# Performance work log

Hardware: AMD Instinct MI355X
Metric: run time of the kernel (lower is better)

Reference implementation:

```python
import jax, jax.numpy as jnp
import numpy as np

EMBED = 256

def _resize(x, h, w):
    # bilinear, half-pixel centers == torch align_corners=False
    B, C = x.shape[:2]
    return jax.image.resize(x, (B, C, h, w), method='bilinear')

def _conv(x, w, b, pad):
    y = jax.lax.conv_general_dilated(x, w, (1, 1), [(pad, pad), (pad, pad)],
                                     dimension_numbers=('NCHW', 'OIHW', 'NCHW'))
    return y + b[None, :, None, None]

def _box1d(x, r, axis):
    # windowed sum over [i-r, i+r], window clipped at borders
    x = jnp.moveaxis(x, axis, -1)
    n = x.shape[-1]
    c = jnp.cumsum(x, axis=-1)
    idx = jnp.arange(n)
    hi = c[..., jnp.clip(idx + r, 0, n - 1)]
    lo_i = idx - r - 1
    lo = jnp.where(lo_i >= 0, c[..., jnp.clip(lo_i, 0, n - 1)], 0.0)
    return jnp.moveaxis(hi - lo, -1, axis)

def _box_mean(x, r):
    # mean filter over (2r+1)^2 window, normalized by valid pixel count at borders
    H, W = x.shape[-2:]
    s = _box1d(_box1d(x, r, -2), r, -1)
    ch = _box1d(jnp.ones((H,), x.dtype), r, 0)
    cw = _box1d(jnp.ones((W,), x.dtype), r, 0)
    return s / (ch[:, None] * cw[None, :])

def _guided_filter(I, p, r, eps):
    # He et al. guided filter. I: (H,W) guide, p: (C,H,W) src, vectorized over C
    mean_I = _box_mean(I, r)
    var_I = _box_mean(I * I, r) - mean_I ** 2
    mean_p = _box_mean(p, r)
    cov_Ip = _box_mean(I[None] * p, r) - mean_I[None] * mean_p
    a = cov_Ip / (var_I[None] + eps)
    b = mean_p - a * mean_I[None]
    return _box_mean(a, r) * I[None] + _box_mean(b, r)

def _forward(fg, bg, mask, feat, w1, b1, w2, b2, w3, b3, wm, bm):
    h2, w2d = 2 * mask.shape[2], 2 * mask.shape[3]
    mask_2x_raw = _resize(mask, h2, w2d)
    feat_2x_raw = _resize(feat, h2, w2d)
    fg_2x = _resize(fg, h2, w2d)
    bg_2x = _resize(bg, h2, w2d)
    x = jnp.concatenate((mask_2x_raw, fg_2x, bg_2x, feat_2x_raw), axis=1)
    x = jax.nn.relu(_conv(x, w1, b1, 0))
    feat_2x = jax.nn.relu(_conv(x, w2, b2, 2))
    guide = jnp.mean(fg_2x, axis=1)[0] * 128.0  # (H2, W2)
    r = int(0.01 * h2)  # static shape -> python int, jit-safe
    filt = _guided_filter(guide, feat_2x[0], r, 0.01)[None]  # (1,C,H2,W2)
    feat_2x = jax.nn.relu(_conv(filt, w3, b3, 0))
    mask_2x = jax.nn.sigmoid(_conv(feat_2x, wm, bm, 0))
    return mask_2x, feat_2x

def setup_inputs():
    key = jax.random.key(0)
    ks = jax.random.split(key, 8)
    E = EMBED
    return {
        'fg': jax.random.normal(ks[0], (1, 3, 128, 128), jnp.float32),
        'bg': jax.random.normal(ks[1], (1, 3, 128, 128), jnp.float32),
        'mask': jax.random.uniform(ks[2], (1, 1, 128, 128), dtype=jnp.float32),
        'feat': jax.random.normal(ks[3], (1, E, 128, 128), jnp.float32),
        'w1': jax.random.normal(ks[4], (E, E + 7, 1, 1), jnp.float32) * 0.05,
        'b1': jnp.zeros((E,), jnp.float32),
        'w2': jax.random.normal(ks[5], (E, E, 5, 5), jnp.float32) * 0.02,
        'b2': jnp.zeros((E,), jnp.float32),
        'w3': jax.random.normal(ks[6], (E, E, 1, 1), jnp.float32) * 0.05,
        'b3': jnp.zeros((E,), jnp.float32),
        'wm': jax.random.normal(ks[7], (1, E, 1, 1), jnp.float32) * 0.05,
        'bm': jnp.zeros((1,), jnp.float32),
    }

def reference(fg, bg, mask, feat, w1, b1, w2, b2, w3, b3, wm, bm):
    return _forward(fg, bg, mask, feat, w1, b1, w2, b2, w3, b3, wm, bm)
```

## Files before the change

### kernel.cpp

```cpp
#include <hip/hip_runtime.h>
#include <hip/hip_bf16.h>
#include <hip/hip_fp16.h>
#include <math.h>


#define P2 65536
#define PADW 260

typedef short  frag8  __attribute__((ext_vector_type(8)));
typedef float  f32x4  __attribute__((ext_vector_type(4)));

__device__ __forceinline__ void load16_lds(const void* gsrc, void* lds) {
    __builtin_amdgcn_global_load_lds((const __attribute__((address_space(1))) void*)gsrc,
                                     (__attribute__((address_space(3))) void*)lds, 16, 0, 0);
}

struct BilC { int y0, y1, x0, x1; float wy0, wy1, wx0, wx1; };
__device__ __forceinline__ BilC bil_coords(int oy, int ox) {
    BilC c;
    int m = oy >> 1;
    if ((oy & 1) == 0) { c.y0 = (m > 0) ? m - 1 : 0; c.y1 = m; c.wy0 = 0.25f; }
    else               { c.y0 = m; c.y1 = (m < 127) ? m + 1 : 127; c.wy0 = 0.75f; }
    c.wy1 = 1.0f - c.wy0;
    int n = ox >> 1;
    if ((ox & 1) == 0) { c.x0 = (n > 0) ? n - 1 : 0; c.x1 = n; c.wx0 = 0.25f; }
    else               { c.x0 = n; c.x1 = (n < 127) ? n + 1 : 127; c.wx0 = 0.75f; }
    c.wx1 = 1.0f - c.wx0;
    return c;
}
__device__ __forceinline__ float bil_eval(const float* __restrict__ src, const BilC& c) {
    return c.wy0 * (c.wx0 * src[c.y0 * 128 + c.x0] + c.wx1 * src[c.y0 * 128 + c.x1])
         + c.wy1 * (c.wx0 * src[c.y1 * 128 + c.x0] + c.wx1 * src[c.y1 * 128 + c.x1]);
}

__global__ void upsample_x(const float* __restrict__ mask, const float* __restrict__ fg,
                           const float* __restrict__ bg, const float* __restrict__ feat,
                           __hip_bfloat16* __restrict__ xp) {
    int p = blockIdx.x * 256 + threadIdx.x;
    int chunk = blockIdx.y;
    union { __hip_bfloat16 h[8]; f32x4 v; } u;
    if (chunk >= 33) {
        f32x4 z = {0.f, 0.f, 0.f, 0.f};
        *(f32x4*)&xp[((size_t)chunk * P2 + p) * 8] = z;
        return;
    }
    BilC bc = bil_coords(p >> 8, p & 255);
#pragma unroll
    for (int j = 0; j < 8; j++) {
        int c = chunk * 8 + j;
        float v = 0.f;
        if (c < 263) {
            const float* src = (c == 0) ? mask
                             : (c < 4)  ? fg + (c - 1) * 16384
                             : (c < 7)  ? bg + (c - 4) * 16384
                             :            feat + (c - 7) * 16384;
            v = bil_eval(src, bc);
        }
        u.h[j] = __float2bfloat16(v);
    }
    *(f32x4*)&xp[((size_t)chunk * P2 + p) * 8] = u.v;
}

__global__ __launch_bounds__(256) void guide_stats(const float* __restrict__ fg,
                                                   float* __restrict__ guide,
                                                   float* __restrict__ meanI,
                                                   float* __restrict__ varI) {
    __shared__ float G[20 * 21];
    int tid = threadIdx.x;
    int gx0 = blockIdx.x * 16, gy0 = blockIdx.y * 16;
    for (int i = tid; i < 400; i += 256) {
        int r = i / 20, c = i - r * 20;
        int gy = gy0 + r - 2, gx = gx0 + c - 2;
        float v = 0.f;
        if ((unsigned)gy < 256u && (unsigned)gx < 256u) {
            BilC bc = bil_coords(gy, gx);
            v = (bil_eval(fg, bc) + bil_eval(fg + 16384, bc) + bil_eval(fg + 32768, bc))
                * (128.0f / 3.0f);
        }
        G[r * 21 + c] = v;
    }
    __syncthreads();
    int ty = tid >> 4, tx = tid & 15;
    int gy = gy0 + ty, gx = gx0 + tx;
    float s = 0.f, ss = 0.f;
#pragma unroll
    for (int dy = 0; dy < 5; dy++)
#pragma unroll
        for (int dx = 0; dx < 5; dx++) {
            float v = G[(ty + dy) * 21 + tx + dx];
            s += v; ss += v * v;
        }
    int cy = ((gy + 2 < 255) ? gy + 2 : 255) - ((gy - 2 > 0) ? gy - 2 : 0) + 1;
    int cx = ((gx + 2 < 255) ? gx + 2 : 255) - ((gx - 2 > 0) ? gx - 2 : 0) + 1;
    float inv = 1.0f / (float)(cy * cx);
    float m = s * inv;
    guide[gy * 256 + gx] = G[(ty + 2) * 21 + tx + 2];
    meanI[gy * 256 + gx] = m;
    varI[gy * 256 + gx]  = ss * inv - m * m;
}

__global__ void prep_all(const float* __restrict__ w2, const float* __restrict__ w1,
                         const float* __restrict__ w3,
                         __hip_bfloat16* __restrict__ wpk2, __hip_bfloat16* __restrict__ wpk1,
                         __hip_bfloat16* __restrict__ wpk3, __hip_bfloat16* __restrict__ y1p,
                         float* __restrict__ haccum) {
    int b = blockIdx.x;
    int tid = threadIdx.x;
    if (b < 129) {
        int idx = b * 256 + tid;
        if (idx >= 33024) return;
        int pid = idx >> 4, chunk = idx & 15;
        int py, px;
        if (pid < 520)       { py = pid / 260;               px = pid - (py) * 260; }
        else if (pid < 1040) { int t = pid - 520; int r = t / 260; py = 258 + r; px = t - r * 260; }
        else                 { int t = pid - 1040; int r = t >> 2; int c = t & 3;
                               py = 2 + r; px = (c < 2) ? c : 256 + c; }
        f32x4 z = {0.f, 0.f, 0.f, 0.f};
        f32x4* dst = (f32x4*)&y1p[((size_t)py * PADW + px) * 256 + chunk * 16];
        dst[0] = z; dst[1] = z;
    } else if (b < 193) {
        int idx = (b - 193 + 64) * 256 + tid - 64 * 256;
        idx = (b - 129) * 256 + tid;
        f32x4 z = {0.f, 0.f, 0.f, 0.f};
        *(f32x4*)&haccum[idx * 4] = z;
    } else if (b < 993) {
        int idx = (b - 193) * 256 + tid;
        int lane = idx & 63;
        int nb = (idx >> 6) & 15;
        int t2 = idx >> 10;
        int tap = t2 % 25, ict = t2 / 25;
        int oc = nb * 16 + (lane & 15);
        int ic0 = ict * 32 + (lane >> 4) * 8;
        union { __hip_bfloat16 h[8]; f32x4 v; } u;
#pragma unroll
        for (int j = 0; j < 8; j++)
            u.h[j] = __float2bfloat16(w2[(oc * 256 + ic0 + j) * 25 + tap]);
        *(f32x4*)&wpk2[(size_t)idx * 8] = u.v;
    } else {
        const float* W; __hip_bfloat16* dst; int K, KT, idx;
        if (b < 1029) { W = w1; dst = wpk1; K = 263; KT = 9; idx = (b - 993) * 256 + tid; }
        else          { W = w3; dst = wpk3; K = 256; KT = 8; idx = (b - 1029) * 256 + tid; }
        if (idx >= KT * 16 * 64) return;
        int lane = idx & 63;
        int nbg = (idx >> 6) & 15;
        int kt = idx >> 10;
        int oc = nbg * 16 + (lane & 15);
        int ic0 = kt * 32 + (lane >> 4) * 8;
        union { __hip_bfloat16 h[8]; f32x4 v; } u;
#pragma unroll
        for (int j = 0; j < 8; j++) {
            int ic = ic0 + j;
            u.h[j] = (ic < K) ? __float2bfloat16(W[(size_t)oc * K + ic]) : __float2bfloat16(0.f);
        }
        *(f32x4*)&dst[(size_t)idx * 8] = u.v;
    }
}

template<int MODE>
__global__ __launch_bounds__(256) void mfma_1x1(const __hip_bfloat16* __restrict__ xch,
                                                const __hip_bfloat16* __restrict__ wpk,
                                                const float* __restrict__ bias,
                                                void* __restrict__ outp, int KT,
                                                const float* __restrict__ wmv,
                                                float* __restrict__ haccum) {
    __shared__ __align__(16) char smem[MODE == 0 ? 34816 : 32768];
    __hip_bfloat16* Asm0 = (__hip_bfloat16*)smem;
    __hip_bfloat16* Bsm0 = (__hip_bfloat16*)(smem + 16384);
    const int tid = threadIdx.x;
    const int wave = tid >> 6, lane = tid & 63;
    const int q = lane >> 4, m16 = lane & 15;
    const int wm = wave & 1, wn = wave >> 1;
    const int pb = blockIdx.x * 128, oh = blockIdx.y;

    f32x4 acc[4][4] = {};

    auto stA = [&](int kt, int buf) {
#pragma unroll
        for (int it = 0; it < 2; it++) {
            int chb = it * 256 + wave * 64;
            int ch = chb + lane;
            int px = ch >> 2, oct = ch & 3;
            const __hip_bfloat16* src = xch + ((size_t)(kt * 4 + oct) * P2 + pb + px) * 8;
            load16_lds(src, &Asm0[(size_t)buf * 4096 + chb * 8]);
        }
    };
    auto stB = [&](int kt, int buf) {
#pragma unroll
        for (int it = 0; it < 2; it++) {
            int chb = it * 256 + wave * 64;
            int ch = chb + lane;
            int nb = ch >> 6, l = ch & 63;
            const __hip_bfloat16* src = wpk + (((size_t)kt * 16 + oh * 8 + nb) * 64 + l) * 8;
            load16_lds(src, &Bsm0[(size_t)buf * 4096 + chb * 8]);
        }
    };
    stA(0, 0); stB(0, 0);
    int buf = 0;
    for (int kt = 0; kt < KT; kt++) {
        __syncthreads();
        if (kt + 1 < KT) { stA(kt + 1, buf ^ 1); stB(kt + 1, buf ^ 1); }
        frag8 a[4], b[4];
#pragma unroll
        for (int i = 0; i < 4; i++)
            a[i] = *(const frag8*)&Asm0[(size_t)buf * 4096 + ((wm * 4 + i) * 16 + m16) * 32 + q * 8];
#pragma unroll
        for (int j = 0; j < 4; j++)
            b[j] = *(const frag8*)&Bsm0[(size_t)buf * 4096 + ((wn * 4 + j) * 64 + lane) * 8];
#pragma unroll
        for (int i = 0; i < 4; i++)
#pragma unroll
            for (int j = 0; j < 4; j++)
                acc[i][j] = __builtin_amdgcn_mfma_f32_16x16x32_bf16(a[i], b[j], acc[i][j], 0, 0, 0);
        buf ^= 1;
    }
    if (MODE == 0) {
        __syncthreads();
        __hip_bfloat16* Ct = (__hip_bfloat16*)smem;
#pragma unroll
        for (int j = 0; j < 4; j++) {
            int ocr = (wn * 4 + j) * 16 + m16;
            float bj = bias[oh * 128 + ocr];
#pragma unroll
            for (int i = 0; i < 4; i++) {
                f32x4 v = acc[i][j];
#pragma unroll
                for (int e = 0; e < 4; e++) {
                    int pxr = (wm * 4 + i) * 16 + q * 4 + e;
                    float tv = v[e] + bj;
                    Ct[pxr * 136 + ocr] = __float2bfloat16(tv > 0.f ? tv : 0.f);
                }
            }
        }
        __syncthreads();
        __hip_bfloat16* y1p = (__hip_bfloat16*)outp;
        int colr = (tid & 15) * 8;
#pragma unroll
        for (int it = 0; it < 8; it++) {
            int pxr = it * 16 + (tid >> 4);
            int pix = pb + pxr;
            int py = pix >> 8, px = pix & 255;
            f32x4 val = *(f32x4*)&Ct[pxr * 136 + colr];
            *(f32x4*)&y1p[((size_t)(py + 2) * PADW + px + 2) * 256 + oh * 128 + colr] = val;
        }
    } else {
        float* outf = (float*)outp;
        float hpart[4][4] = {};
#pragma unroll
        for (int j = 0; j < 4; j++) {
            int oc = oh * 128 + (wn * 4 + j) * 16 + m16;
            float bj = bias[oc];
            float wj = wmv[oc];
#pragma unroll
            for (int i = 0; i < 4; i++) {
                f32x4 v = acc[i][j];
#pragma unroll
                for (int e = 0; e < 4; e++) {
                    float tv = v[e] + bj;
                    tv = tv > 0.f ? tv : 0.f;
                    v[e] = tv;
                    hpart[i][e] += wj * tv;
                }
                *(f32x4*)&outf[(size_t)oc * P2 + pb + (wm * 4 + i) * 16 + q * 4] = v;
            }
        }
#pragma unroll
        for (int i = 0; i < 4; i++)
#pragma unroll
            for (int e = 0; e < 4; e++) {
                float s = hpart[i][e];
                s += __shfl_xor(s, 1);
                s += __shfl_xor(s, 2);
                s += __shfl_xor(s, 4);
                s += __shfl_xor(s, 8);
                if (m16 == 0)
                    atomicAdd(&haccum[pb + (wm * 4 + i) * 16 + q * 4 + e], s);
            }
    }
}

__global__ __launch_bounds__(128, 2) void conv5x5_mfma(const __hip_bfloat16* __restrict__ y1p,
                                                       const __hip_bfloat16* __restrict__ wpk,
                                                       const float* __restrict__ bias,
                                                       __half* __restrict__ pf) {
    __shared__ __align__(16) __hip_bfloat16 Asm[2][12 * 20 * 32];
    const int tid = threadIdx.x;
    const int wave = tid >> 6;
    const int lane = tid & 63;
    const int q = lane >> 4;
    const int m16 = lane & 15;
    const int bx = blockIdx.x, by = blockIdx.y, oh = blockIdx.z;

    f32x4 acc[4][8] = {};

    auto stageA = [&](int ict, int buf) {
#pragma unroll
        for (int g = 0; g < 8; g++) {
            int grp = g * 2 + wave;
            if (grp >= 15) break;
            int chb = grp * 64;
            int ch = chb + lane;
            int oct = ch & 3, pl = ch >> 2;
            int pc = pl % 20, pr = pl / 20;
            const __hip_bfloat16* src =
                y1p + (size_t)((by * 8 + pr) * PADW + bx * 16 + pc) * 256 + ict * 32 + oct * 8;
            load16_lds(src, &Asm[buf][chb * 8]);
        }
    };

    const __hip_bfloat16* bptr = wpk + ((size_t)(oh * 8) * 64 + lane) * 8;
    frag8 b[2][8];
    auto loadB = [&](frag8* dst) {
#pragma unroll
        for (int j = 0; j < 8; j++)
            dst[j] = *(const frag8*)(bptr + j * 512);
        bptr += 8192;
    };

    stageA(0, 0);
    loadB(b[0]);
    int abuf = 0;

    for (int ict = 0; ict < 8; ict++) {
        __syncthreads();
        const __hip_bfloat16* aptr = &Asm[abuf][(wave * 80 + m16) * 32 + q * 8];
#pragma unroll
        for (int tap = 0; tap < 25; tap++) {
            const int dy = tap / 5, dx = tap % 5;
            if (tap < 24) loadB(b[(tap + 1) & 1]);
            else if (ict < 7) stageA(ict + 1, abuf ^ 1);
            frag8 a[4];
#pragma unroll
            for (int i = 0; i < 4; i++)
                a[i] = *(const frag8*)(aptr + ((i + dy) * 20 + dx) * 32);
            frag8* bc = b[tap & 1];
#pragma unroll
            for (int i = 0; i < 4; i++)
#pragma unroll
                for (int j = 0; j < 8; j++)
                    acc[i][j] = __builtin_amdgcn_mfma_f32_16x16x32_bf16(a[i], bc[j], acc[i][j], 0, 0, 0);
            if (tap == 24 && ict < 7) loadB(b[0]);
        }
        abuf ^= 1;
    }

#pragma unroll
    for (int j = 0; j < 8; j++) {
        int oc = oh * 128 + j * 16 + m16;
        float bj = bias[oc];
#pragma unroll
        for (int i = 0; i < 4; i++) {
            int r = wave * 4 + i;
            f32x4 v = acc[i][j];
            union { __half h[4]; double d; } u;
#pragma unroll
            for (int e = 0; e < 4; e++) {
                float t = v[e] + bj;
                u.h[e] = __float2half(t > 0.f ? t : 0.f);
            }
            *(double*)&pf[(size_t)oc * P2 + (by * 8 + r) * 256 + bx * 16 + q * 4] = u.d;
        }
    }
}

__global__ __launch_bounds__(256) void gf_stream(const __half* __restrict__ p,
                                                 const float* __restrict__ guide,
                                                 const float* __restrict__ meanI,
                                                 const float* __restrict__ varI,
                                                 __hip_bfloat16* __restrict__ filt) {
    __shared__ float Prow[260], IProw[260], Arow[260], Brow[260];
    const int t = threadIdx.x;
    const int c = blockIdx.y;
    const int Y0 = blockIdx.x * 64;
    const __half* pc = p + (size_t)c * P2;
    if (t < 4) {
        int e = (t < 2) ? t : 256 + t;
        Prow[e] = 0.f; IProw[e] = 0.f; Arow[e] = 0.f; Brow[e] = 0.f;
    }
    int xlo = (t - 2 > 0) ? t - 2 : 0, xhi = (t + 2 < 255) ? t + 2 : 255;
    const float cxr = 1.0f / (float)(xhi - xlo + 1);
    float hp[5] = {0, 0, 0, 0, 0}, hip[5] = {0, 0, 0, 0, 0};
    float ha[5] = {0, 0, 0, 0, 0}, hb[5] = {0, 0, 0, 0, 0};
    float vp = 0.f, vip = 0.f, va = 0.f, vb = 0.f;
    __syncthreads();
    for (int s = 0; s < 72; s++) {
        int yL = Y0 - 4 + s;
        bool okL = ((unsigned)yL < 256u);
        if (okL) {
            float pv = __half2float(pc[yL * 256 + t]);
            Prow[t + 2] = pv;
            IProw[t + 2] = guide[yL * 256 + t] * pv;
        }
        __syncthreads();
        float hpn = 0.f, hipn = 0.f;
        if (okL) {
            hpn  = Prow[t] + Prow[t + 1] + Prow[t + 2] + Prow[t + 3] + Prow[t + 4];
            hipn = IProw[t] + IProw[t + 1] + IProw[t + 2] + IProw[t + 3] + IProw[t + 4];
        }
        vp += hpn - hp[0];  vip += hipn - hip[0];
        hp[0] = hp[1]; hp[1] = hp[2]; hp[2] = hp[3]; hp[3] = hp[4]; hp[4] = hpn;
        hip[0] = hip[1]; hip[1] = hip[2]; hip[2] = hip[3]; hip[3] = hip[4]; hip[4] = hipn;
        int yA = yL - 2;
        float aV = 0.f, bV = 0.f;
        if ((unsigned)yA < 256u && yA >= Y0 - 2) {
            int ylo = (yA - 2 > 0) ? yA - 2 : 0, yhi = (yA + 2 < 255) ? yA + 2 : 255;
            float inv1 = cxr / (float)(yhi - ylo + 1);
            float mI = meanI[yA * 256 + t], vI = varI[yA * 256 + t];
            float mp = vp * inv1, mip = vip * inv1;
            float cov = mip - mI * mp;
            aV = cov / (vI + 0.01f);
            bV = mp - aV * mI;
        }
        Arow[t + 2] = aV;
        Brow[t + 2] = bV;
        __syncthreads();
        float han = Arow[t] + Arow[t + 1] + Arow[t + 2] + Arow[t + 3] + Arow[t + 4];
        float hbn = Brow[t] + Brow[t + 1] + Brow[t + 2] + Brow[t + 3] + Brow[t + 4];
        va += han - ha[0];  vb += hbn - hb[0];
        ha[0] = ha[1]; ha[1] = ha[2]; ha[2] = ha[3]; ha[3] = ha[4]; ha[4] = han;
        hb[0] = hb[1]; hb[1] = hb[2]; hb[2] = hb[3]; hb[3] = hb[4]; hb[4] = hbn;
        int yo = yL - 4;
        if (yo >= Y0 && yo < Y0 + 64 && (unsigned)yo < 256u) {
            int ylo = (yo - 2 > 0) ? yo - 2 : 0, yhi = (yo + 2 < 255) ? yo + 2 : 255;
            float inv2 = cxr / (float)(yhi - ylo + 1);
            float I = guide[yo * 256 + t];
            filt[(size_t)c * P2 + yo * 256 + t] = __float2bfloat16((va * I + vb) * inv2);
        }
    }
}

__global__ void transpose_cp(const __hip_bfloat16* __restrict__ filt,
                             __hip_bfloat16* __restrict__ filtp) {
    __shared__ __hip_bfloat16 T[8][1032];
    int tid = threadIdx.x;
    int p0 = blockIdx.x * 1024;
    int cg = blockIdx.y;
    for (int i = tid; i < 4096; i += 256) {
        int r = i >> 9, pl2 = (i & 511) * 2;
        unsigned v = *(const unsigned*)&filt[(size_t)(cg * 8 + r) * P2 + p0 + pl2];
        *(unsigned*)&T[r][pl2] = v;
    }
    __syncthreads();
    for (int pl = tid; pl < 1024; pl += 256) {
        union { __hip_bfloat16 h[8]; f32x4 v; } u;
#pragma unroll
        for (int j = 0; j < 8; j++) u.h[j] = T[j][pl];
        *(f32x4*)&filtp[((size_t)cg * P2 + p0 + pl) * 8] = u.v;
    }
}

__global__ void sigmoid_head(const float* __restrict__ haccum, const float* __restrict__ bm,
                             float* __restrict__ out) {
    int p = blockIdx.x * 256 + threadIdx.x;
    out[p] = 1.0f / (1.0f + expf(-(haccum[p] + bm[0])));
}

extern "C" void kernel_launch(void* const* d_in, const int* in_sizes, int n_in,
                              void* d_out, int out_size, void* d_ws, size_t ws_size,
                              hipStream_t stream) {
    const float* fg   = (const float*)d_in[0];
    const float* bg   = (const float*)d_in[1];
    const float* mask = (const float*)d_in[2];
    const float* feat = (const float*)d_in[3];
    const float* w1   = (const float*)d_in[4];
    const float* b1   = (const float*)d_in[5];
    const float* w2   = (const float*)d_in[6];
    const float* b2   = (const float*)d_in[7];
    const float* w3   = (const float*)d_in[8];
    const float* b3   = (const float*)d_in[9];
    const float* wm   = (const float*)d_in[10];
    const float* bm   = (const float*)d_in[11];
    float* out = (float*)d_out;
    char* w8 = (char*)d_ws;

    __half* pbuf          = (__half*)w8;
    __hip_bfloat16* filtp = (__hip_bfloat16*)(w8 + 33554432);
    __hip_bfloat16* xp    = (__hip_bfloat16*)(w8 + 67108864);
    __hip_bfloat16* filt  = (__hip_bfloat16*)(w8 + 67108864);
    __hip_bfloat16* y1p   = (__hip_bfloat16*)(w8 + 104857600);
    __hip_bfloat16* wpk2  = (__hip_bfloat16*)(w8 + 139468800);
    __hip_bfloat16* wpk1  = (__hip_bfloat16*)(w8 + 142745600);
    __hip_bfloat16* wpk3  = (__hip_bfloat16*)(w8 + 142893056);
    float* guide  = (float*)(w8 + 143024128);
    float* meanI  = guide + P2;
    float* varI   = meanI + P2;
    float* haccum = varI + P2;

    upsample_x<<<dim3(256, 36), 256, 0, stream>>>(mask, fg, bg, feat, xp);
    guide_stats<<<dim3(16, 16), 256, 0, stream>>>(fg, guide, meanI, varI);
    prep_all<<<1061, 256, 0, stream>>>(w2, w1, w3, wpk2, wpk1, wpk3, y1p, haccum);
    mfma_1x1<0><<<dim3(512, 2), 256, 0, stream>>>(xp, wpk1, b1, y1p, 9, nullptr, nullptr);
    conv5x5_mfma<<<dim3(16, 32, 2), 128, 0, stream>>>(y1p, wpk2, b2, pbuf);
    gf_stream<<<dim3(4, 256), 256, 0, stream>>>(pbuf, guide, meanI, varI, filt);
    transpose_cp<<<dim3(64, 32), 256, 0, stream>>>(filt, filtp);
    mfma_1x1<1><<<dim3(512, 2), 256, 0, stream>>>(filtp, wpk3, b3, out + P2, 8, wm, haccum);
    sigmoid_head<<<256, 256, 0, stream>>>(haccum, bm, out);
}
```

Measured before the change: 444.8 us.

## Compute all output channels per block in 1x1 convs and reorder conv5x5 weight packing

```diff
diff --git a/kernel.cpp b/kernel.cpp
--- a/kernel.cpp
+++ b/kernel.cpp
@@ -119,22 +119,21 @@
         f32x4* dst = (f32x4*)&y1p[((size_t)py * PADW + px) * 256 + chunk * 16];
         dst[0] = z; dst[1] = z;
     } else if (b < 193) {
-        int idx = (b - 193 + 64) * 256 + tid - 64 * 256;
-        idx = (b - 129) * 256 + tid;
+        int idx = (b - 129) * 256 + tid;
         f32x4 z = {0.f, 0.f, 0.f, 0.f};
         *(f32x4*)&haccum[idx * 4] = z;
     } else if (b < 993) {
         int idx = (b - 193) * 256 + tid;
         int lane = idx & 63;
         int nb = (idx >> 6) & 15;
-        int t2 = idx >> 10;
-        int tap = t2 % 25, ict = t2 / 25;
+        int kt = (idx >> 10) & 7;
+        int t  = idx >> 13;
         int oc = nb * 16 + (lane & 15);
-        int ic0 = ict * 32 + (lane >> 4) * 8;
+        int ic0 = kt * 32 + (lane >> 4) * 8;
         union { __hip_bfloat16 h[8]; f32x4 v; } u;
 #pragma unroll
         for (int j = 0; j < 8; j++)
-            u.h[j] = __float2bfloat16(w2[(oc * 256 + ic0 + j) * 25 + tap]);
+            u.h[j] = __float2bfloat16(w2[(oc * 256 + ic0 + j) * 25 + t]);
         *(f32x4*)&wpk2[(size_t)idx * 8] = u.v;
     } else {
         const float* W; __hip_bfloat16* dst; int K, KT, idx;
@@ -163,16 +162,16 @@
                                                 void* __restrict__ outp, int KT,
                                                 const float* __restrict__ wmv,
                                                 float* __restrict__ haccum) {
-    __shared__ __align__(16) char smem[MODE == 0 ? 34816 : 32768];
+    __shared__ __align__(16) char smem[MODE == 0 ? 67584 : 49152];
     __hip_bfloat16* Asm0 = (__hip_bfloat16*)smem;
     __hip_bfloat16* Bsm0 = (__hip_bfloat16*)(smem + 16384);
     const int tid = threadIdx.x;
     const int wave = tid >> 6, lane = tid & 63;
     const int q = lane >> 4, m16 = lane & 15;
-    const int wm = wave & 1, wn = wave >> 1;
-    const int pb = blockIdx.x * 128, oh = blockIdx.y;
-
-    f32x4 acc[4][4] = {};
+    const int wn = wave;
+    const int pb = blockIdx.x * 128;
+
+    f32x4 acc[8][4] = {};
 
     auto stA = [&](int kt, int buf) {
 #pragma unroll
@@ -186,12 +185,12 @@
     };
     auto stB = [&](int kt, int buf) {
 #pragma unroll
-        for (int it = 0; it < 2; it++) {
+        for (int it = 0; it < 4; it++) {
             int chb = it * 256 + wave * 64;
             int ch = chb + lane;
             int nb = ch >> 6, l = ch & 63;
-            const __hip_bfloat16* src = wpk + (((size_t)kt * 16 + oh * 8 + nb) * 64 + l) * 8;
-            load16_lds(src, &Bsm0[(size_t)buf * 4096 + chb * 8]);
+            const __hip_bfloat16* src = wpk + (((size_t)kt * 16 + nb) * 64 + l) * 8;
+            load16_lds(src, &Bsm0[(size_t)buf * 8192 + chb * 8]);
         }
     };
     stA(0, 0); stB(0, 0);
@@ -199,15 +198,15 @@
     for (int kt = 0; kt < KT; kt++) {
         __syncthreads();
         if (kt + 1 < KT) { stA(kt + 1, buf ^ 1); stB(kt + 1, buf ^ 1); }
-        frag8 a[4], b[4];
-#pragma unroll
-        for (int i = 0; i < 4; i++)
-            a[i] = *(const frag8*)&Asm0[(size_t)buf * 4096 + ((wm * 4 + i) * 16 + m16) * 32 + q * 8];
+        frag8 a[8], b[4];
+#pragma unroll
+        for (int i = 0; i < 8; i++)
+            a[i] = *(const frag8*)&Asm0[(size_t)buf * 4096 + (i * 16 + m16) * 32 + q * 8];
 #pragma unroll
         for (int j = 0; j < 4; j++)
-            b[j] = *(const frag8*)&Bsm0[(size_t)buf * 4096 + ((wn * 4 + j) * 64 + lane) * 8];
-#pragma unroll
-        for (int i = 0; i < 4; i++)
+            b[j] = *(const frag8*)&Bsm0[(size_t)buf * 8192 + ((wn * 4 + j) * 64 + lane) * 8];
+#pragma unroll
+        for (int i = 0; i < 8; i++)
 #pragma unroll
             for (int j = 0; j < 4; j++)
                 acc[i][j] = __builtin_amdgcn_mfma_f32_16x16x32_bf16(a[i], b[j], acc[i][j], 0, 0, 0);
@@ -219,39 +218,39 @@
 #pragma unroll
         for (int j = 0; j < 4; j++) {
             int ocr = (wn * 4 + j) * 16 + m16;
-            float bj = bias[oh * 128 + ocr];
-#pragma unroll
-            for (int i = 0; i < 4; i++) {
+            float bj = bias[ocr];
+#pragma unroll
+            for (int i = 0; i < 8; i++) {
                 f32x4 v = acc[i][j];
 #pragma unroll
                 for (int e = 0; e < 4; e++) {
-                    int pxr = (wm * 4 + i) * 16 + q * 4 + e;
+                    int pxr = i * 16 + q * 4 + e;
                     float tv = v[e] + bj;
-                    Ct[pxr * 136 + ocr] = __float2bfloat16(tv > 0.f ? tv : 0.f);
+                    Ct[pxr * 264 + ocr] = __float2bfloat16(tv > 0.f ? tv : 0.f);
                 }
             }
         }
         __syncthreads();
         __hip_bfloat16* y1p = (__hip_bfloat16*)outp;
-        int colr = (tid & 15) * 8;
-#pragma unroll
-        for (int it = 0; it < 8; it++) {
-            int pxr = it * 16 + (tid >> 4);
+        int colr = (tid & 31) * 8;
+#pragma unroll
+        for (int it = 0; it < 16; it++) {
+            int pxr = it * 8 + (tid >> 5);
             int pix = pb + pxr;
             int py = pix >> 8, px = pix & 255;
-            f32x4 val = *(f32x4*)&Ct[pxr * 136 + colr];
-            *(f32x4*)&y1p[((size_t)(py + 2) * PADW + px + 2) * 256 + oh * 128 + colr] = val;
+            f32x4 val = *(f32x4*)&Ct[pxr * 264 + colr];
+            *(f32x4*)&y1p[((size_t)(py + 2) * PADW + px + 2) * 256 + colr] = val;
         }
     } else {
         float* outf = (float*)outp;
-        float hpart[4][4] = {};
+        float hpart[8][4] = {};
 #pragma unroll
         for (int j = 0; j < 4; j++) {
-            int oc = oh * 128 + (wn * 4 + j) * 16 + m16;
+            int oc = (wn * 4 + j) * 16 + m16;
             float bj = bias[oc];
             float wj = wmv[oc];
 #pragma unroll
-            for (int i = 0; i < 4; i++) {
+            for (int i = 0; i < 8; i++) {
                 f32x4 v = acc[i][j];
 #pragma unroll
                 for (int e = 0; e < 4; e++) {
@@ -260,11 +259,11 @@
                     v[e] = tv;
                     hpart[i][e] += wj * tv;
                 }
-                *(f32x4*)&outf[(size_t)oc * P2 + pb + (wm * 4 + i) * 16 + q * 4] = v;
+                *(f32x4*)&outf[(size_t)oc * P2 + pb + i * 16 + q * 4] = v;
             }
         }
 #pragma unroll
-        for (int i = 0; i < 4; i++)
+        for (int i = 0; i < 8; i++)
 #pragma unroll
             for (int e = 0; e < 4; e++) {
                 float s = hpart[i][e];
@@ -273,7 +272,7 @@
                 s += __shfl_xor(s, 4);
                 s += __shfl_xor(s, 8);
                 if (m16 == 0)
-                    atomicAdd(&haccum[pb + (wm * 4 + i) * 16 + q * 4 + e], s);
+                    atomicAdd(&haccum[pb + i * 16 + q * 4 + e], s);
             }
     }
 }
@@ -306,42 +305,38 @@
             load16_lds(src, &Asm[buf][chb * 8]);
         }
     };
-
-    const __hip_bfloat16* bptr = wpk + ((size_t)(oh * 8) * 64 + lane) * 8;
-    frag8 b[2][8];
-    auto loadB = [&](frag8* dst) {
+    auto loadB = [&](int s, frag8* dst) {
+        int ict = s / 25, tap = s - ict * 25;
+        const __hip_bfloat16* base =
+            wpk + ((size_t)((tap * 8 + ict) * 16 + oh * 8) * 64 + lane) * 8;
 #pragma unroll
         for (int j = 0; j < 8; j++)
-            dst[j] = *(const frag8*)(bptr + j * 512);
-        bptr += 8192;
+            dst[j] = *(const frag8*)(base + (size_t)j * 512);
     };
 
+    frag8 bA[8], bB[8];
     stageA(0, 0);
-    loadB(b[0]);
+    loadB(0, bA);
     int abuf = 0;
 
-    for (int ict = 0; ict < 8; ict++) {
-        __syncthreads();
-        const __hip_bfloat16* aptr = &Asm[abuf][(wave * 80 + m16) * 32 + q * 8];
-#pragma unroll
-        for (int tap = 0; tap < 25; tap++) {
-            const int dy = tap / 5, dx = tap % 5;
-            if (tap < 24) loadB(b[(tap + 1) & 1]);
-            else if (ict < 7) stageA(ict + 1, abuf ^ 1);
-            frag8 a[4];
-#pragma unroll
-            for (int i = 0; i < 4; i++)
-                a[i] = *(const frag8*)(aptr + ((i + dy) * 20 + dx) * 32);
-            frag8* bc = b[tap & 1];
-#pragma unroll
-            for (int i = 0; i < 4; i++)
-#pragma unroll
-                for (int j = 0; j < 8; j++)
-                    acc[i][j] = __builtin_amdgcn_mfma_f32_16x16x32_bf16(a[i], bc[j], acc[i][j], 0, 0, 0);
-            if (tap == 24 && ict < 7) loadB(b[0]);
-        }
-        abuf ^= 1;
-    }
+    auto step = [&](int s, frag8* bcur, frag8* bnxt) {
+        int ict = s / 25, tap = s - ict * 25;
+        if (tap == 0) __syncthreads();
+        if (s + 1 < 200) loadB(s + 1, bnxt);
+        if (tap == 24 && ict < 7) stageA(ict + 1, abuf ^ 1);
+        int dy = tap / 5, dx = tap - dy * 5;
+        frag8 a[4];
+#pragma unroll
+        for (int i = 0; i < 4; i++)
+            a[i] = *(const frag8*)&Asm[abuf][((wave * 4 + i + dy) * 20 + m16 + dx) * 32 + q * 8];
+#pragma unroll
+        for (int i = 0; i < 4; i++)
+#pragma unroll
+            for (int j = 0; j < 8; j++)
+                acc[i][j] = __builtin_amdgcn_mfma_f32_16x16x32_bf16(a[i], bcur[j], acc[i][j], 0, 0, 0);
+        if (tap == 24) abuf ^= 1;
+    };
+    for (int s = 0; s < 200; s += 2) { step(s, bA, bB); step(s + 1, bB, bA); }
 
 #pragma unroll
     for (int j = 0; j < 8; j++) {
@@ -488,10 +483,10 @@
     upsample_x<<<dim3(256, 36), 256, 0, stream>>>(mask, fg, bg, feat, xp);
     guide_stats<<<dim3(16, 16), 256, 0, stream>>>(fg, guide, meanI, varI);
     prep_all<<<1061, 256, 0, stream>>>(w2, w1, w3, wpk2, wpk1, wpk3, y1p, haccum);
-    mfma_1x1<0><<<dim3(512, 2), 256, 0, stream>>>(xp, wpk1, b1, y1p, 9, nullptr, nullptr);
+    mfma_1x1<0><<<512, 256, 0, stream>>>(xp, wpk1, b1, y1p, 9, nullptr, nullptr);
     conv5x5_mfma<<<dim3(16, 32, 2), 128, 0, stream>>>(y1p, wpk2, b2, pbuf);
     gf_stream<<<dim3(4, 256), 256, 0, stream>>>(pbuf, guide, meanI, varI, filt);
     transpose_cp<<<dim3(64, 32), 256, 0, stream>>>(filt, filtp);
-    mfma_1x1<1><<<dim3(512, 2), 256, 0, stream>>>(filtp, wpk3, b3, out + P2, 8, wm, haccum);
+    mfma_1x1<1><<<512, 256, 0, stream>>>(filtp, wpk3, b3, out + P2, 8, wm, haccum);
     sigmoid_head<<<256, 256, 0, stream>>>(haccum, bm, out);
 }
```

Result: faster. 434.2 us (-2.4%).
